# Optimization experiments

Measured on AMD Instinct MI355X. Metric: run time of the kernel, lower is better.

Reference implementation:

```python
import jax, jax.numpy as jnp
import numpy as np
import math

D_MODEL, H, D_FF = 1024, 16, 4096
B, S = 4, 2048
EPS = 1e-6

def layer_norm(x, alpha, beta):
    # Faithful to torch: x.std uses Bessel correction (ddof=1), eps added to std.
    mean = jnp.mean(x, axis=-1, keepdims=True)
    std = jnp.std(x, axis=-1, keepdims=True, ddof=1)
    return alpha * (x - mean) / (std + EPS) + beta

def setup_inputs() -> dict:
    key = jax.random.key(0)
    ks = jax.random.split(key, 8)
    sc = 0.02
    return {
        "x": jax.random.normal(ks[0], (B, S, D_MODEL), jnp.float32),
        "mask": jnp.ones((B, 1, 1, S), jnp.int32),
        "wq": jax.random.normal(ks[1], (D_MODEL, D_MODEL), jnp.float32) * sc,
        "wk": jax.random.normal(ks[2], (D_MODEL, D_MODEL), jnp.float32) * sc,
        "wv": jax.random.normal(ks[3], (D_MODEL, D_MODEL), jnp.float32) * sc,
        "wo": jax.random.normal(ks[4], (D_MODEL, D_MODEL), jnp.float32) * sc,
        "w1": jax.random.normal(ks[5], (D_MODEL, D_FF), jnp.float32) * sc,
        "b1": jnp.zeros((D_FF,), jnp.float32),
        "w2": jax.random.normal(ks[6], (D_FF, D_MODEL), jnp.float32) * sc,
        "b2": jnp.zeros((D_MODEL,), jnp.float32),
        "ln1_a": jnp.ones((D_MODEL,), jnp.float32),
        "ln1_b": jnp.zeros((D_MODEL,), jnp.float32),
        "ln2_a": jnp.ones((D_MODEL,), jnp.float32),
        "ln2_b": jnp.zeros((D_MODEL,), jnp.float32),
    }

def mha(xn, mask, wq, wk, wv, wo):
    b, s, d = xn.shape
    d_k = d // H
    q = (xn @ wq).reshape(b, s, H, d_k).transpose(0, 2, 1, 3)  # [B,H,S,dk]
    k = (xn @ wk).reshape(b, s, H, d_k).transpose(0, 2, 1, 3)
    v = (xn @ wv).reshape(b, s, H, d_k).transpose(0, 2, 1, 3)
    scores = jnp.einsum('bhqd,bhkd->bhqk', q, k) / math.sqrt(d_k)
    scores = jnp.where(mask == 0, -1e9, scores)
    attn = jax.nn.softmax(scores, axis=-1)
    out = jnp.einsum('bhqk,bhkd->bhqd', attn, v)
    out = out.transpose(0, 2, 1, 3).reshape(b, s, d)
    return out @ wo

def reference(x, mask, wq, wk, wv, wo, w1, b1, w2, b2, ln1_a, ln1_b, ln2_a, ln2_b):
    # Pre-LN residual 1: self-attention (dropout=0 / eval mode -> identity)
    xn = layer_norm(x, ln1_a, ln1_b)
    x = x + mha(xn, mask, wq, wk, wv, wo)
    # Pre-LN residual 2: FFN
    xn = layer_norm(x, ln2_a, ln2_b)
    ff = jax.nn.relu(xn @ w1 + b1) @ w2 + b2
    return x + ff
```

## Files before the change

### kernel.cpp

```cpp
#include <hip/hip_runtime.h>
#include <hip/hip_bf16.h>

typedef __bf16 bf16x8 __attribute__((ext_vector_type(8)));
typedef __bf16 bf16x4 __attribute__((ext_vector_type(4)));
typedef float  f32x4  __attribute__((ext_vector_type(4)));

#define MFMA(a, b, c) __builtin_amdgcn_mfma_f32_16x16x32_bf16((a), (b), (c), 0, 0, 0)

#define GLOAD16(gp, lp) __builtin_amdgcn_global_load_lds(                      \
    (const __attribute__((address_space(1))) void*)(gp),                       \
    (__attribute__((address_space(3))) void*)(lp), 16, 0, 0)

__device__ inline unsigned int pkbf(float a, float b) {
    __bf16 x = (__bf16)a, y = (__bf16)b;
    return (unsigned int)*(unsigned short*)&x |
           ((unsigned int)*(unsigned short*)&y << 16);
}

__global__ __launch_bounds__(256) void transpose_cvt(
    const float* __restrict__ src, __bf16* __restrict__ dst, int Kd, int Nd)
{
    __shared__ float tile[32][33];
    const int k0 = blockIdx.y * 32, n0 = blockIdx.x * 32;
    const int t = threadIdx.x;
    const int r = t >> 5, c = t & 31;
#pragma unroll
    for (int i = 0; i < 4; ++i)
        tile[r + i * 8][c] = src[(long)(k0 + r + i * 8) * Nd + n0 + c];
    __syncthreads();
#pragma unroll
    for (int i = 0; i < 4; ++i)
        dst[(long)(n0 + r + i * 8) * Kd + k0 + c] = (__bf16)tile[c][r + i * 8];
}

__global__ __launch_bounds__(256) void transpose_v(
    const __bf16* __restrict__ V, __bf16* __restrict__ Vt)
{
    __shared__ __bf16 tile[32][33];
    const int bh = blockIdx.z;
    const int s0 = blockIdx.x * 32, d0 = blockIdx.y * 32;
    const int t = threadIdx.x, r = t >> 5, c = t & 31;
    const __bf16* Vp = V + (long)bh * 2048 * 64;
    __bf16* Tp = Vt + (long)bh * 64 * 2048;
#pragma unroll
    for (int i = 0; i < 4; ++i)
        tile[r + i * 8][c] = Vp[(long)(s0 + r + i * 8) * 64 + d0 + c];
    __syncthreads();
#pragma unroll
    for (int i = 0; i < 4; ++i)
        Tp[(long)(d0 + r + i * 8) * 2048 + s0 + c] = tile[c][r + i * 8];
}

__global__ __launch_bounds__(256) void ln_kernel(
    const float* __restrict__ in, const float* __restrict__ ga,
    const float* __restrict__ gb, __bf16* __restrict__ out)
{
    const int row = blockIdx.x;
    const int t = threadIdx.x;
    const float4 xv = *(const float4*)(in + (long)row * 1024 + t * 4);
    float s  = xv.x + xv.y + xv.z + xv.w;
    float sq = xv.x * xv.x + xv.y * xv.y + xv.z * xv.z + xv.w * xv.w;
#pragma unroll
    for (int off = 32; off; off >>= 1) {
        s  += __shfl_xor(s, off);
        sq += __shfl_xor(sq, off);
    }
    __shared__ float red[8];
    const int w = t >> 6;
    if ((t & 63) == 0) { red[w * 2] = s; red[w * 2 + 1] = sq; }
    __syncthreads();
    s  = red[0] + red[2] + red[4] + red[6];
    sq = red[1] + red[3] + red[5] + red[7];
    const float mean = s * (1.0f / 1024.0f);
    const float var  = fmaxf((sq - s * mean) * (1.0f / 1023.0f), 0.0f);
    const float dinv = 1.0f / (sqrtf(var) + 1e-6f);
    const float4 av = *(const float4*)(ga + t * 4);
    const float4 bv = *(const float4*)(gb + t * 4);
    bf16x4 o;
    o[0] = (__bf16)((xv.x - mean) * dinv * av.x + bv.x);
    o[1] = (__bf16)((xv.y - mean) * dinv * av.y + bv.y);
    o[2] = (__bf16)((xv.z - mean) * dinv * av.z + bv.z);
    o[3] = (__bf16)((xv.w - mean) * dinv * av.w + bv.w);
    *(bf16x4*)(out + (long)row * 1024 + t * 4) = o;
}

template <int MODE>
__global__ __launch_bounds__(256) void gemm_bt(
    const __bf16* __restrict__ A, const __bf16* __restrict__ Bt,
    int M, int N, int K,
    const float* __restrict__ bias, const float* resid,
    float* outf, __bf16* __restrict__ outb,
    __bf16* __restrict__ qb, __bf16* __restrict__ kb, __bf16* __restrict__ vb)
{
    __shared__ __align__(16) __bf16 Alds[128 * 32];
    __shared__ __align__(16) __bf16 Blds[128 * 32];

    const int t = threadIdx.x;
    const int lane = t & 63, w = t >> 6;
    const int wr = w >> 1, wc = w & 1;
    const int g = lane >> 4, l15 = lane & 15;

    const int nwg = gridDim.x * gridDim.y;
    const int hwid = blockIdx.y * gridDim.x + blockIdx.x;
    const int wid = (hwid & 7) * (nwg >> 3) + (hwid >> 3);
    const int bm = (wid / gridDim.x) * 128;
    const int bn = (wid % gridDim.x) * 128;

    const int cr = t >> 2;
    const int cc = (t & 3) * 8;
    const __bf16* Ag  = A  + (long)(bm + cr) * K + cc;
    const __bf16* Ag2 = Ag + (long)64 * K;
    const __bf16* Bg  = Bt + (long)(bn + cr) * K + cc;
    const __bf16* Bg2 = Bg + (long)64 * K;
    char* Alp = (char*)Alds + t * 16;
    char* Blp = (char*)Blds + t * 16;

    f32x4 acc[4][4] = {};
    const int nk = K / 32;

    for (int kt = 0; kt < nk; ++kt) {
        const long ko = (long)kt * 32;
        __syncthreads();
        GLOAD16(Ag + ko,  Alp);
        GLOAD16(Ag2 + ko, Alp + 4096);
        GLOAD16(Bg + ko,  Blp);
        GLOAD16(Bg2 + ko, Blp + 4096);
        __syncthreads();
        bf16x8 af[4], bfr[4];
#pragma unroll
        for (int mi = 0; mi < 4; ++mi)
            af[mi] = *(const bf16x8*)(Alds + (wr * 64 + mi * 16 + l15) * 32 + g * 8);
#pragma unroll
        for (int ni = 0; ni < 4; ++ni)
            bfr[ni] = *(const bf16x8*)(Blds + (wc * 64 + ni * 16 + l15) * 32 + g * 8);
#pragma unroll
        for (int mi = 0; mi < 4; ++mi)
#pragma unroll
            for (int ni = 0; ni < 4; ++ni)
                acc[mi][ni] = MFMA(af[mi], bfr[ni], acc[mi][ni]);
    }

#pragma unroll
    for (int mi = 0; mi < 4; ++mi) {
#pragma unroll
        for (int ni = 0; ni < 4; ++ni) {
#pragma unroll
            for (int r = 0; r < 4; ++r) {
                const int gr = bm + wr * 64 + mi * 16 + g * 4 + r;
                const int gc = bn + wc * 64 + ni * 16 + l15;
                const float vacc = acc[mi][ni][r];
                if constexpr (MODE == 0) {
                    const int bufi = gc >> 10;
                    const int hd = gc & 1023;
                    const int h = hd >> 6, d = hd & 63;
                    const int b = gr >> 11, sx = gr & 2047;
                    __bf16* dst = (bufi == 0) ? qb : ((bufi == 1) ? kb : vb);
                    dst[((long)((b * 16 + h) * 2048 + sx)) * 64 + d] = (__bf16)vacc;
                } else if constexpr (MODE == 1) {
                    const long idx = (long)gr * N + gc;
                    outf[idx] = vacc + resid[idx];
                } else if constexpr (MODE == 2) {
                    const float y = fmaxf(vacc + bias[gc], 0.0f);
                    outb[(long)gr * N + gc] = (__bf16)y;
                } else {
                    const long idx = (long)gr * N + gc;
                    outf[idx] = vacc + bias[gc] + resid[idx];
                }
            }
        }
    }
}

__global__ __launch_bounds__(256, 2) void attn_kernel(
    const __bf16* __restrict__ Q, const __bf16* __restrict__ Kk,
    const __bf16* __restrict__ Vt, const int* __restrict__ mask,
    __bf16* __restrict__ O)
{
    __shared__ __align__(16) char Klds[8192];
    __shared__ __align__(16) char Vlds[8192];
    __shared__ int mlds[64];
    __shared__ int tflag[32];

    const int t = threadIdx.x;
    const int lane = t & 63, w = t >> 6;
    const int g = lane >> 4, l15 = lane & 15;
    const int bh = blockIdx.x >> 4;
    const int qt = blockIdx.x & 15;
    const int b = bh >> 4, h = bh & 15;
    const int q0 = qt * 128 + w * 32;

    const __bf16* Qp = Q  + (long)bh * 2048 * 64;
    const __bf16* Kp = Kk + (long)bh * 2048 * 64;
    const __bf16* Vp = Vt + (long)bh * 64 * 2048;
    const int* mp = mask + b * 2048;

    {
        const int4* mi4 = (const int4*)(mp + t * 8);
        const int4 ma = mi4[0], mb = mi4[1];
        const int ok = (ma.x && ma.y && ma.z && ma.w &&
                        mb.x && mb.y && mb.z && mb.w) ? 1 : 0;
        const unsigned long long bal = __ballot(ok);
        if ((lane & 7) == 0)
            tflag[t >> 3] = (((bal >> lane) & 0xFFull) == 0xFFull) ? 1 : 0;
    }

    bf16x8 qreg[2][2];
#pragma unroll
    for (int qf = 0; qf < 2; ++qf)
#pragma unroll
        for (int kh = 0; kh < 2; ++kh)
            qreg[qf][kh] = *(const bf16x8*)(Qp + (long)(q0 + qf * 16 + l15) * 64 + kh * 32 + g * 8);

    bf16x8 vone;
#pragma unroll
    for (int j = 0; j < 8; ++j) vone[j] = (__bf16)1.0f;

    const float Csc = 0.18033688011112042f;
    float m2_run[2] = {-1e30f, -1e30f};
    f32x4 la[2] = {};
    f32x4 ot[2][4] = {};

    const int sr0 = t >> 3;
    const int sce = (t & 7) * 8;
    const int swz0 = sr0 * 128 + (((t & 7) * 16) ^ ((sr0 & 7) << 4));
    const int swz1 = swz0 + 32 * 128;

    bf16x8 kr0 = *(const bf16x8*)(Kp + (long)sr0 * 64 + sce);
    bf16x8 kr1 = *(const bf16x8*)(Kp + (long)(sr0 + 32) * 64 + sce);
    bf16x8 vr0 = *(const bf16x8*)(Vp + (long)sr0 * 2048 + sce);
    bf16x8 vr1 = *(const bf16x8*)(Vp + (long)(sr0 + 32) * 2048 + sce);
    int mr = (t < 64) ? mp[t] : 0;

    for (int kc = 0; kc < 32; ++kc) {
        __syncthreads();
        *(bf16x8*)(Klds + swz0) = kr0;
        *(bf16x8*)(Klds + swz1) = kr1;
        *(bf16x8*)(Vlds + swz0) = vr0;
        *(bf16x8*)(Vlds + swz1) = vr1;
        if (t < 64) mlds[t] = mr;
        __syncthreads();
        if (kc < 31) {
            const int kv0 = (kc + 1) * 64;
            kr0 = *(const bf16x8*)(Kp + (long)(kv0 + sr0) * 64 + sce);
            kr1 = *(const bf16x8*)(Kp + (long)(kv0 + sr0 + 32) * 64 + sce);
            vr0 = *(const bf16x8*)(Vp + (long)sr0 * 2048 + kv0 + sce);
            vr1 = *(const bf16x8*)(Vp + (long)(sr0 + 32) * 2048 + kv0 + sce);
            if (t < 64) mr = mp[kv0 + t];
        }
        const bool fullv = (tflag[kc] != 0);

        bf16x8 kf[4][2];
#pragma unroll
        for (int f = 0; f < 4; ++f)
#pragma unroll
            for (int dh = 0; dh < 2; ++dh)
                kf[f][dh] = *(const bf16x8*)(Klds + (f * 16 + l15) * 128 +
                                             ((dh * 64 + g * 16) ^ ((l15 & 7) << 4)));
        f32x4 sf[2][4] = {};
        __builtin_amdgcn_s_setprio(1);
#pragma unroll
        for (int qf = 0; qf < 2; ++qf)
#pragma unroll
            for (int f = 0; f < 4; ++f) {
                sf[qf][f] = MFMA(kf[f][0], qreg[qf][0], sf[qf][f]);
                sf[qf][f] = MFMA(kf[f][1], qreg[qf][1], sf[qf][f]);
            }
        __builtin_amdgcn_s_setprio(0);

        bf16x8 av[4][2];
#pragma unroll
        for (int df = 0; df < 4; ++df) {
            const int row = (df * 16 + l15) * 128;
            const int sx = (l15 & 7) << 4;
#pragma unroll
            for (int hh = 0; hh < 2; ++hh) {
                const bf16x4 lo = *(const bf16x4*)(Vlds + row + ((hh * 64 + g * 8) ^ sx));
                const bf16x4 hi = *(const bf16x4*)(Vlds + row + ((hh * 64 + 32 + g * 8) ^ sx));
                bf16x8 a;
                a[0] = lo[0]; a[1] = lo[1]; a[2] = lo[2]; a[3] = lo[3];
                a[4] = hi[0]; a[5] = hi[1]; a[6] = hi[2]; a[7] = hi[3];
                av[df][hh] = a;
            }
        }

#pragma unroll
        for (int qf = 0; qf < 2; ++qf) {
            float s[16];
            if (fullv) {
#pragma unroll
                for (int i = 0; i < 16; ++i) s[i] = sf[qf][i >> 2][i & 3];
            } else {
                int mvv[16];
#pragma unroll
                for (int f = 0; f < 4; ++f) {
                    const int4 mq = *(const int4*)&mlds[f * 16 + g * 4];
                    mvv[f * 4 + 0] = mq.x; mvv[f * 4 + 1] = mq.y;
                    mvv[f * 4 + 2] = mq.z; mvv[f * 4 + 3] = mq.w;
                }
#pragma unroll
                for (int i = 0; i < 16; ++i)
                    s[i] = (mvv[i] == 0) ? -1e9f : sf[qf][i >> 2][i & 3];
            }
            float m01 = fmaxf(s[0], s[1]),   m23 = fmaxf(s[2], s[3]);
            float m45 = fmaxf(s[4], s[5]),   m67 = fmaxf(s[6], s[7]);
            float m89 = fmaxf(s[8], s[9]),   mab = fmaxf(s[10], s[11]);
            float mcd = fmaxf(s[12], s[13]), mef = fmaxf(s[14], s[15]);
            float mx = fmaxf(fmaxf(fmaxf(m01, m23), fmaxf(m45, m67)),
                             fmaxf(fmaxf(m89, mab), fmaxf(mcd, mef)));
            mx = fmaxf(mx, __shfl_xor(mx, 16));
            mx = fmaxf(mx, __shfl_xor(mx, 32));
            const float m2 = mx * Csc;
            if (!__all(m2 - m2_run[qf] <= 8.0f)) {
                const float m2n = fmaxf(m2_run[qf], m2);
                const float alpha = __builtin_amdgcn_exp2f(m2_run[qf] - m2n);
#pragma unroll
                for (int r = 0; r < 4; ++r) la[qf][r] *= alpha;
#pragma unroll
                for (int df = 0; df < 4; ++df)
#pragma unroll
                    for (int r = 0; r < 4; ++r) ot[qf][df][r] *= alpha;
                m2_run[qf] = m2n;
            }
            const float nm2 = -m2_run[qf];
            float p[16];
#pragma unroll
            for (int i = 0; i < 16; ++i)
                p[i] = __builtin_amdgcn_exp2f(__builtin_fmaf(s[i], Csc, nm2));

#pragma unroll
            for (int hh = 0; hh < 2; ++hh) {
                unsigned int pu[4] = {pkbf(p[hh * 8 + 0], p[hh * 8 + 1]),
                                      pkbf(p[hh * 8 + 2], p[hh * 8 + 3]),
                                      pkbf(p[hh * 8 + 4], p[hh * 8 + 5]),
                                      pkbf(p[hh * 8 + 6], p[hh * 8 + 7])};
                bf16x8 pf = *(bf16x8*)pu;
                __builtin_amdgcn_s_setprio(1);
#pragma unroll
                for (int df = 0; df < 4; ++df)
                    ot[qf][df] = MFMA(av[df][hh], pf, ot[qf][df]);
                la[qf] = MFMA(vone, pf, la[qf]);
                __builtin_amdgcn_s_setprio(0);
            }
        }
    }

#pragma unroll
    for (int qf = 0; qf < 2; ++qf) {
        const float inv = 1.0f / la[qf][0];
        const int q = q0 + qf * 16 + l15;
        __bf16* orow = O + (long)(b * 2048 + q) * 1024 + h * 64;
#pragma unroll
        for (int df = 0; df < 4; ++df)
#pragma unroll
            for (int rp = 0; rp < 2; ++rp) {
                const int d = df * 16 + g * 4 + rp * 2;
                *(unsigned int*)(orow + d) =
                    pkbf(ot[qf][df][rp * 2] * inv, ot[qf][df][rp * 2 + 1] * inv);
            }
    }
}

extern "C" void kernel_launch(void* const* d_in, const int* in_sizes, int n_in,
                              void* d_out, int out_size, void* d_ws, size_t ws_size,
                              hipStream_t stream)
{
    const float* x    = (const float*)d_in[0];
    const int*   mask = (const int*)  d_in[1];
    const float* wq   = (const float*)d_in[2];
    const float* wk   = (const float*)d_in[3];
    const float* wv   = (const float*)d_in[4];
    const float* wo   = (const float*)d_in[5];
    const float* w1   = (const float*)d_in[6];
    const float* b1   = (const float*)d_in[7];
    const float* w2   = (const float*)d_in[8];
    const float* b2   = (const float*)d_in[9];
    const float* l1a  = (const float*)d_in[10];
    const float* l1b  = (const float*)d_in[11];
    const float* l2a  = (const float*)d_in[12];
    const float* l2b  = (const float*)d_in[13];
    float* out = (float*)d_out;

    char* ws = (char*)d_ws;
    __bf16* wqkvT = (__bf16*)(ws);
    __bf16* woT   = (__bf16*)(ws + 6291456);
    __bf16* w1T   = (__bf16*)(ws + 8388608);
    __bf16* w2T   = (__bf16*)(ws + 16777216);
    __bf16* xn    = (__bf16*)(ws + 25165824);
    __bf16* Vtb   = (__bf16*)(ws + 25165824);
    __bf16* Qb    = (__bf16*)(ws + 41943040);
    __bf16* Kb    = (__bf16*)(ws + 58720256);
    __bf16* Vb    = (__bf16*)(ws + 75497472);
    __bf16* attO  = (__bf16*)(ws + 92274688);
    __bf16* ffh   = (__bf16*)(ws + 41943040);

    transpose_cvt<<<dim3(32, 32),  256, 0, stream>>>(wq, wqkvT,               1024, 1024);
    transpose_cvt<<<dim3(32, 32),  256, 0, stream>>>(wk, wqkvT + 1024 * 1024, 1024, 1024);
    transpose_cvt<<<dim3(32, 32),  256, 0, stream>>>(wv, wqkvT + 2048 * 1024, 1024, 1024);
    transpose_cvt<<<dim3(32, 32),  256, 0, stream>>>(wo, woT,                 1024, 1024);
    transpose_cvt<<<dim3(128, 32), 256, 0, stream>>>(w1, w1T,                 1024, 4096);
    transpose_cvt<<<dim3(32, 128), 256, 0, stream>>>(w2, w2T,                 4096, 1024);

    ln_kernel<<<8192, 256, 0, stream>>>(x, l1a, l1b, xn);
    gemm_bt<0><<<dim3(24, 64), 256, 0, stream>>>(xn, wqkvT, 8192, 3072, 1024,
                                                 nullptr, nullptr, nullptr, nullptr, Qb, Kb, Vb);
    transpose_v<<<dim3(64, 2, 64), 256, 0, stream>>>(Vb, Vtb);
    attn_kernel<<<1024, 256, 0, stream>>>(Qb, Kb, Vtb, mask, attO);
    gemm_bt<1><<<dim3(8, 64), 256, 0, stream>>>(attO, woT, 8192, 1024, 1024,
                                                nullptr, x, out, nullptr, nullptr, nullptr, nullptr);
    ln_kernel<<<8192, 256, 0, stream>>>(out, l2a, l2b, xn);
    gemm_bt<2><<<dim3(32, 64), 256, 0, stream>>>(xn, w1T, 8192, 4096, 1024,
                                                 b1, nullptr, nullptr, ffh, nullptr, nullptr, nullptr);
    gemm_bt<3><<<dim3(8, 64), 256, 0, stream>>>(ffh, w2T, 8192, 1024, 4096,
                                                b2, out, out, nullptr, nullptr, nullptr, nullptr);
    (void)in_sizes; (void)n_in; (void)out_size; (void)ws_size;
}
```

Measured before the change: 490.8 us.

## Double-buffer LDS tiles in GEMM and attention kernels with explicit waitcnt barriers

The GEMM main loop now uses two LDS buffers and prefetches tile kt+2 via global_load_lds while computing on the current tile. It uses explicit vmcnt/lgkmcnt waits and raw s_barrier in place of two __syncthreads per iteration, and raises wave priority around the MFMAs. The attention kernel also double-buffers its K/V/mask LDS tiles, so the next tile is written to the alternate buffer after compute, leaving one barrier per iteration. The goal is to overlap global memory latency with MFMA work and cut barrier stalls, at the cost of twice the LDS. That could lower occupancy, and the hand-written waitcnt logic is fragile.

Result: slower. 516.0 us (+5.1%).

```diff
diff --git a/kernel.cpp b/kernel.cpp
--- a/kernel.cpp
+++ b/kernel.cpp
@@ -10,6 +10,13 @@
 #define GLOAD16(gp, lp) __builtin_amdgcn_global_load_lds(                      \
     (const __attribute__((address_space(1))) void*)(gp),                       \
     (__attribute__((address_space(3))) void*)(lp), 16, 0, 0)
+
+#define WAITV4() asm volatile("s_waitcnt vmcnt(4)" ::: "memory")
+#define WAITV0() asm volatile("s_waitcnt vmcnt(0)" ::: "memory")
+#define WAITL()  asm volatile("s_waitcnt lgkmcnt(0)" ::: "memory")
+#define SBAR()   do { __builtin_amdgcn_sched_barrier(0);                       \
+                      __builtin_amdgcn_s_barrier();                            \
+                      __builtin_amdgcn_sched_barrier(0); } while (0)
 
 __device__ inline unsigned int pkbf(float a, float b) {
     __bf16 x = (__bf16)a, y = (__bf16)b;
@@ -92,8 +99,8 @@
     float* outf, __bf16* __restrict__ outb,
     __bf16* __restrict__ qb, __bf16* __restrict__ kb, __bf16* __restrict__ vb)
 {
-    __shared__ __align__(16) __bf16 Alds[128 * 32];
-    __shared__ __align__(16) __bf16 Blds[128 * 32];
+    __shared__ __align__(16) __bf16 Alds[2][128 * 32];
+    __shared__ __align__(16) __bf16 Blds[2][128 * 32];
 
     const int t = threadIdx.x;
     const int lane = t & 63, w = t >> 6;
@@ -112,33 +119,55 @@
     const __bf16* Ag2 = Ag + (long)64 * K;
     const __bf16* Bg  = Bt + (long)(bn + cr) * K + cc;
     const __bf16* Bg2 = Bg + (long)64 * K;
-    char* Alp = (char*)Alds + t * 16;
-    char* Blp = (char*)Blds + t * 16;
+    char* Alp = (char*)(&Alds[0][0]) + t * 16;
+    char* Blp = (char*)(&Blds[0][0]) + t * 16;
 
     f32x4 acc[4][4] = {};
     const int nk = K / 32;
 
+#define STAGE_T(kt, buf) do {                                                  \
+        const long ko_ = (long)(kt) * 32;                                      \
+        GLOAD16(Ag  + ko_, Alp + (buf) * 8192);                                \
+        GLOAD16(Ag2 + ko_, Alp + (buf) * 8192 + 4096);                         \
+        GLOAD16(Bg  + ko_, Blp + (buf) * 8192);                                \
+        GLOAD16(Bg2 + ko_, Blp + (buf) * 8192 + 4096); } while (0)
+
+    STAGE_T(0, 0);
+    STAGE_T(1, 1);
+    WAITV4();
+    SBAR();
+
     for (int kt = 0; kt < nk; ++kt) {
-        const long ko = (long)kt * 32;
-        __syncthreads();
-        GLOAD16(Ag + ko,  Alp);
-        GLOAD16(Ag2 + ko, Alp + 4096);
-        GLOAD16(Bg + ko,  Blp);
-        GLOAD16(Bg2 + ko, Blp + 4096);
-        __syncthreads();
+        const int cur = kt & 1;
+        const __bf16* Ab = &Alds[cur][0];
+        const __bf16* Bb = &Blds[cur][0];
         bf16x8 af[4], bfr[4];
 #pragma unroll
         for (int mi = 0; mi < 4; ++mi)
-            af[mi] = *(const bf16x8*)(Alds + (wr * 64 + mi * 16 + l15) * 32 + g * 8);
+            af[mi] = *(const bf16x8*)(Ab + (wr * 64 + mi * 16 + l15) * 32 + g * 8);
 #pragma unroll
         for (int ni = 0; ni < 4; ++ni)
-            bfr[ni] = *(const bf16x8*)(Blds + (wc * 64 + ni * 16 + l15) * 32 + g * 8);
+            bfr[ni] = *(const bf16x8*)(Bb + (wc * 64 + ni * 16 + l15) * 32 + g * 8);
+        __builtin_amdgcn_s_setprio(1);
 #pragma unroll
         for (int mi = 0; mi < 4; ++mi)
 #pragma unroll
             for (int ni = 0; ni < 4; ++ni)
                 acc[mi][ni] = MFMA(af[mi], bfr[ni], acc[mi][ni]);
-    }
+        __builtin_amdgcn_s_setprio(0);
+        WAITL();
+        SBAR();
+        if (kt + 1 < nk) {
+            if (kt + 2 < nk) {
+                STAGE_T(kt + 2, cur);
+                WAITV4();
+            } else {
+                WAITV0();
+            }
+            SBAR();
+        }
+    }
+#undef STAGE_T
 
 #pragma unroll
     for (int mi = 0; mi < 4; ++mi) {
@@ -176,9 +205,9 @@
     const __bf16* __restrict__ Vt, const int* __restrict__ mask,
     __bf16* __restrict__ O)
 {
-    __shared__ __align__(16) char Klds[8192];
-    __shared__ __align__(16) char Vlds[8192];
-    __shared__ int mlds[64];
+    __shared__ __align__(16) char Klds[2][8192];
+    __shared__ __align__(16) char Vlds[2][8192];
+    __shared__ int mlds[2][64];
     __shared__ int tflag[32];
 
     const int t = threadIdx.x;
@@ -230,23 +259,23 @@
     bf16x8 vr0 = *(const bf16x8*)(Vp + (long)sr0 * 2048 + sce);
     bf16x8 vr1 = *(const bf16x8*)(Vp + (long)(sr0 + 32) * 2048 + sce);
     int mr = (t < 64) ? mp[t] : 0;
+    *(bf16x8*)(Klds[0] + swz0) = kr0;
+    *(bf16x8*)(Klds[0] + swz1) = kr1;
+    *(bf16x8*)(Vlds[0] + swz0) = vr0;
+    *(bf16x8*)(Vlds[0] + swz1) = vr1;
+    if (t < 64) mlds[0][t] = mr;
+    kr0 = *(const bf16x8*)(Kp + (long)(64 + sr0) * 64 + sce);
+    kr1 = *(const bf16x8*)(Kp + (long)(64 + sr0 + 32) * 64 + sce);
+    vr0 = *(const bf16x8*)(Vp + (long)sr0 * 2048 + 64 + sce);
+    vr1 = *(const bf16x8*)(Vp + (long)(sr0 + 32) * 2048 + 64 + sce);
+    mr = (t < 64) ? mp[64 + t] : 0;
+    WAITL();
+    SBAR();
 
     for (int kc = 0; kc < 32; ++kc) {
-        __syncthreads();
-        *(bf16x8*)(Klds + swz0) = kr0;
-        *(bf16x8*)(Klds + swz1) = kr1;
-        *(bf16x8*)(Vlds + swz0) = vr0;
-        *(bf16x8*)(Vlds + swz1) = vr1;
-        if (t < 64) mlds[t] = mr;
-        __syncthreads();
-        if (kc < 31) {
-            const int kv0 = (kc + 1) * 64;
-            kr0 = *(const bf16x8*)(Kp + (long)(kv0 + sr0) * 64 + sce);
-            kr1 = *(const bf16x8*)(Kp + (long)(kv0 + sr0 + 32) * 64 + sce);
-            vr0 = *(const bf16x8*)(Vp + (long)sr0 * 2048 + kv0 + sce);
-            vr1 = *(const bf16x8*)(Vp + (long)(sr0 + 32) * 2048 + kv0 + sce);
-            if (t < 64) mr = mp[kv0 + t];
-        }
+        const int cur = kc & 1;
+        const char* Kc = Klds[cur];
+        const char* Vc = Vlds[cur];
         const bool fullv = (tflag[kc] != 0);
 
         bf16x8 kf[4][2];
@@ -254,7 +283,7 @@
         for (int f = 0; f < 4; ++f)
 #pragma unroll
             for (int dh = 0; dh < 2; ++dh)
-                kf[f][dh] = *(const bf16x8*)(Klds + (f * 16 + l15) * 128 +
+                kf[f][dh] = *(const bf16x8*)(Kc + (f * 16 + l15) * 128 +
                                              ((dh * 64 + g * 16) ^ ((l15 & 7) << 4)));
         f32x4 sf[2][4] = {};
         __builtin_amdgcn_s_setprio(1);
@@ -274,8 +303,8 @@
             const int sx = (l15 & 7) << 4;
 #pragma unroll
             for (int hh = 0; hh < 2; ++hh) {
-                const bf16x4 lo = *(const bf16x4*)(Vlds + row + ((hh * 64 + g * 8) ^ sx));
-                const bf16x4 hi = *(const bf16x4*)(Vlds + row + ((hh * 64 + 32 + g * 8) ^ sx));
+                const bf16x4 lo = *(const bf16x4*)(Vc + row + ((hh * 64 + g * 8) ^ sx));
+                const bf16x4 hi = *(const bf16x4*)(Vc + row + ((hh * 64 + 32 + g * 8) ^ sx));
                 bf16x8 a;
                 a[0] = lo[0]; a[1] = lo[1]; a[2] = lo[2]; a[3] = lo[3];
                 a[4] = hi[0]; a[5] = hi[1]; a[6] = hi[2]; a[7] = hi[3];
@@ -293,7 +322,7 @@
                 int mvv[16];
 #pragma unroll
                 for (int f = 0; f < 4; ++f) {
-                    const int4 mq = *(const int4*)&mlds[f * 16 + g * 4];
+                    const int4 mq = *(const int4*)&mlds[cur][f * 16 + g * 4];
                     mvv[f * 4 + 0] = mq.x; mvv[f * 4 + 1] = mq.y;
                     mvv[f * 4 + 2] = mq.z; mvv[f * 4 + 3] = mq.w;
                 }
@@ -342,6 +371,26 @@
                 __builtin_amdgcn_s_setprio(0);
             }
         }
+
+        if (kc < 31) {
+            char* Kn = Klds[cur ^ 1];
+            char* Vn = Vlds[cur ^ 1];
+            *(bf16x8*)(Kn + swz0) = kr0;
+            *(bf16x8*)(Kn + swz1) = kr1;
+            *(bf16x8*)(Vn + swz0) = vr0;
+            *(bf16x8*)(Vn + swz1) = vr1;
+            if (t < 64) mlds[cur ^ 1][t] = mr;
+            if (kc < 30) {
+                const int kv0 = (kc + 2) * 64;
+                kr0 = *(const bf16x8*)(Kp + (long)(kv0 + sr0) * 64 + sce);
+                kr1 = *(const bf16x8*)(Kp + (long)(kv0 + sr0 + 32) * 64 + sce);
+                vr0 = *(const bf16x8*)(Vp + (long)sr0 * 2048 + kv0 + sce);
+                vr1 = *(const bf16x8*)(Vp + (long)(sr0 + 32) * 2048 + kv0 + sce);
+                mr = (t < 64) ? mp[kv0 + t] : 0;
+            }
+            WAITL();
+        }
+        SBAR();
     }
 
 #pragma unroll
```

## Load attention K/V fragments directly from global memory, dropping LDS staging

Applied to the files above, without the earlier changes.

The attention kernel no longer stages K, V and mask tiles through shared memory with two barriers per key chunk. Each wave now loads its MFMA fragments straight from global memory and relies on L1/L2 for reuse across the four waves. Blocks are also remapped so that neighbouring block IDs fall on different batch-heads, and the occupancy hint in launch_bounds is dropped. The intent is to remove barrier stalls and LDS traffic, at the cost of more global and cache traffic, narrower 8-byte V loads, and no explicit prefetch.

New measurement: 701.9 us. +43.0%, slower.

```diff
diff --git a/kernel.cpp b/kernel.cpp
--- a/kernel.cpp
+++ b/kernel.cpp
@@ -171,21 +171,21 @@
     }
 }
 
-__global__ __launch_bounds__(256, 2) void attn_kernel(
+__global__ __launch_bounds__(256) void attn_kernel(
     const __bf16* __restrict__ Q, const __bf16* __restrict__ Kk,
     const __bf16* __restrict__ Vt, const int* __restrict__ mask,
     __bf16* __restrict__ O)
 {
-    __shared__ __align__(16) char Klds[8192];
-    __shared__ __align__(16) char Vlds[8192];
-    __shared__ int mlds[64];
     __shared__ int tflag[32];
 
     const int t = threadIdx.x;
     const int lane = t & 63, w = t >> 6;
     const int g = lane >> 4, l15 = lane & 15;
-    const int bh = blockIdx.x >> 4;
-    const int qt = blockIdx.x & 15;
+
+    const int bid = blockIdx.x;
+    const int idx = bid >> 3;
+    const int bh = (bid & 7) * 8 + (idx >> 4);
+    const int qt = idx & 15;
     const int b = bh >> 4, h = bh & 15;
     const int q0 = qt * 128 + w * 32;
 
@@ -203,6 +203,7 @@
         if ((lane & 7) == 0)
             tflag[t >> 3] = (((bal >> lane) & 0xFFull) == 0xFFull) ? 1 : 0;
     }
+    __syncthreads();
 
     bf16x8 qreg[2][2];
 #pragma unroll
@@ -220,42 +221,31 @@
     f32x4 la[2] = {};
     f32x4 ot[2][4] = {};
 
-    const int sr0 = t >> 3;
-    const int sce = (t & 7) * 8;
-    const int swz0 = sr0 * 128 + (((t & 7) * 16) ^ ((sr0 & 7) << 4));
-    const int swz1 = swz0 + 32 * 128;
-
-    bf16x8 kr0 = *(const bf16x8*)(Kp + (long)sr0 * 64 + sce);
-    bf16x8 kr1 = *(const bf16x8*)(Kp + (long)(sr0 + 32) * 64 + sce);
-    bf16x8 vr0 = *(const bf16x8*)(Vp + (long)sr0 * 2048 + sce);
-    bf16x8 vr1 = *(const bf16x8*)(Vp + (long)(sr0 + 32) * 2048 + sce);
-    int mr = (t < 64) ? mp[t] : 0;
+    const __bf16* kbase = Kp + (long)l15 * 64 + g * 8;
+    const __bf16* vbase = Vp + (long)l15 * 2048 + g * 4;
 
     for (int kc = 0; kc < 32; ++kc) {
-        __syncthreads();
-        *(bf16x8*)(Klds + swz0) = kr0;
-        *(bf16x8*)(Klds + swz1) = kr1;
-        *(bf16x8*)(Vlds + swz0) = vr0;
-        *(bf16x8*)(Vlds + swz1) = vr1;
-        if (t < 64) mlds[t] = mr;
-        __syncthreads();
-        if (kc < 31) {
-            const int kv0 = (kc + 1) * 64;
-            kr0 = *(const bf16x8*)(Kp + (long)(kv0 + sr0) * 64 + sce);
-            kr1 = *(const bf16x8*)(Kp + (long)(kv0 + sr0 + 32) * 64 + sce);
-            vr0 = *(const bf16x8*)(Vp + (long)sr0 * 2048 + kv0 + sce);
-            vr1 = *(const bf16x8*)(Vp + (long)(sr0 + 32) * 2048 + kv0 + sce);
-            if (t < 64) mr = mp[kv0 + t];
+        const int kv0 = kc * 64;
+        const bool fullv = (tflag[kc] != 0);
+
+        bf16x8 kf[4][2];
+#pragma unroll
+        for (int f = 0; f < 4; ++f)
+#pragma unroll
+            for (int dh = 0; dh < 2; ++dh)
+                kf[f][dh] = *(const bf16x8*)(kbase + (long)(kv0 + f * 16) * 64 + dh * 32);
+
+        bf16x4 avlo[4][2], avhi[4][2];
+#pragma unroll
+        for (int df = 0; df < 4; ++df) {
+            const __bf16* vrow = vbase + (long)(df * 16) * 2048 + kv0;
+#pragma unroll
+            for (int hh = 0; hh < 2; ++hh) {
+                avlo[df][hh] = *(const bf16x4*)(vrow + hh * 32);
+                avhi[df][hh] = *(const bf16x4*)(vrow + hh * 32 + 16);
+            }
         }
-        const bool fullv = (tflag[kc] != 0);
-
-        bf16x8 kf[4][2];
-#pragma unroll
-        for (int f = 0; f < 4; ++f)
-#pragma unroll
-            for (int dh = 0; dh < 2; ++dh)
-                kf[f][dh] = *(const bf16x8*)(Klds + (f * 16 + l15) * 128 +
-                                             ((dh * 64 + g * 16) ^ ((l15 & 7) << 4)));
+
         f32x4 sf[2][4] = {};
         __builtin_amdgcn_s_setprio(1);
 #pragma unroll
@@ -267,22 +257,6 @@
             }
         __builtin_amdgcn_s_setprio(0);
 
-        bf16x8 av[4][2];
-#pragma unroll
-        for (int df = 0; df < 4; ++df) {
-            const int row = (df * 16 + l15) * 128;
-            const int sx = (l15 & 7) << 4;
-#pragma unroll
-            for (int hh = 0; hh < 2; ++hh) {
-                const bf16x4 lo = *(const bf16x4*)(Vlds + row + ((hh * 64 + g * 8) ^ sx));
-                const bf16x4 hi = *(const bf16x4*)(Vlds + row + ((hh * 64 + 32 + g * 8) ^ sx));
-                bf16x8 a;
-                a[0] = lo[0]; a[1] = lo[1]; a[2] = lo[2]; a[3] = lo[3];
-                a[4] = hi[0]; a[5] = hi[1]; a[6] = hi[2]; a[7] = hi[3];
-                av[df][hh] = a;
-            }
-        }
-
 #pragma unroll
         for (int qf = 0; qf < 2; ++qf) {
             float s[16];
@@ -290,16 +264,14 @@
 #pragma unroll
                 for (int i = 0; i < 16; ++i) s[i] = sf[qf][i >> 2][i & 3];
             } else {
-                int mvv[16];
 #pragma unroll
                 for (int f = 0; f < 4; ++f) {
-                    const int4 mq = *(const int4*)&mlds[f * 16 + g * 4];
-                    mvv[f * 4 + 0] = mq.x; mvv[f * 4 + 1] = mq.y;
-                    mvv[f * 4 + 2] = mq.z; mvv[f * 4 + 3] = mq.w;
+                    const int4 mq = *(const int4*)(mp + kv0 + f * 16 + g * 4);
+                    s[f * 4 + 0] = (mq.x == 0) ? -1e9f : sf[qf][f][0];
+                    s[f * 4 + 1] = (mq.y == 0) ? -1e9f : sf[qf][f][1];
+                    s[f * 4 + 2] = (mq.z == 0) ? -1e9f : sf[qf][f][2];
+                    s[f * 4 + 3] = (mq.w == 0) ? -1e9f : sf[qf][f][3];
                 }
-#pragma unroll
-                for (int i = 0; i < 16; ++i)
-                    s[i] = (mvv[i] == 0) ? -1e9f : sf[qf][i >> 2][i & 3];
             }
             float m01 = fmaxf(s[0], s[1]),   m23 = fmaxf(s[2], s[3]);
             float m45 = fmaxf(s[4], s[5]),   m67 = fmaxf(s[6], s[7]);
@@ -336,8 +308,14 @@
                 bf16x8 pf = *(bf16x8*)pu;
                 __builtin_amdgcn_s_setprio(1);
 #pragma unroll
-                for (int df = 0; df < 4; ++df)
-                    ot[qf][df] = MFMA(av[df][hh], pf, ot[qf][df]);
+                for (int df = 0; df < 4; ++df) {
+                    bf16x8 a;
+                    a[0] = avlo[df][hh][0]; a[1] = avlo[df][hh][1];
+                    a[2] = avlo[df][hh][2]; a[3] = avlo[df][hh][3];
+                    a[4] = avhi[df][hh][0]; a[5] = avhi[df][hh][1];
+                    a[6] = avhi[df][hh][2]; a[7] = avhi[df][hh][3];
+                    ot[qf][df] = MFMA(a, pf, ot[qf][df]);
+                }
                 la[qf] = MFMA(vone, pf, la[qf]);
                 __builtin_amdgcn_s_setprio(0);
             }
```

## Double-buffer GEMM LDS tiles with register-staged global prefetch

Applied to the files above, without the earlier changes.

Replaces the direct global-to-LDS loads, which needed two barriers per K step, with register-staged prefetch into a double-buffered LDS tile. The loads for step kt+2 are issued while step kt computes, and the loop now has one barrier per iteration. The aim is to hide global memory latency behind MFMA work. In exchange it doubles LDS use, adds registers for staging, and routes data through VGPRs instead of the direct LDS load path.

Result: faster. 456.4 us (-7.0%).

```diff
diff --git a/kernel.cpp b/kernel.cpp
--- a/kernel.cpp
+++ b/kernel.cpp
@@ -6,10 +6,6 @@
 typedef float  f32x4  __attribute__((ext_vector_type(4)));
 
 #define MFMA(a, b, c) __builtin_amdgcn_mfma_f32_16x16x32_bf16((a), (b), (c), 0, 0, 0)
-
-#define GLOAD16(gp, lp) __builtin_amdgcn_global_load_lds(                      \
-    (const __attribute__((address_space(1))) void*)(gp),                       \
-    (__attribute__((address_space(3))) void*)(lp), 16, 0, 0)
 
 __device__ inline unsigned int pkbf(float a, float b) {
     __bf16 x = (__bf16)a, y = (__bf16)b;
@@ -92,8 +88,8 @@
     float* outf, __bf16* __restrict__ outb,
     __bf16* __restrict__ qb, __bf16* __restrict__ kb, __bf16* __restrict__ vb)
 {
-    __shared__ __align__(16) __bf16 Alds[128 * 32];
-    __shared__ __align__(16) __bf16 Blds[128 * 32];
+    __shared__ __align__(16) __bf16 Alds[2][128 * 32];
+    __shared__ __align__(16) __bf16 Blds[2][128 * 32];
 
     const int t = threadIdx.x;
     const int lane = t & 63, w = t >> 6;
@@ -112,32 +108,55 @@
     const __bf16* Ag2 = Ag + (long)64 * K;
     const __bf16* Bg  = Bt + (long)(bn + cr) * K + cc;
     const __bf16* Bg2 = Bg + (long)64 * K;
-    char* Alp = (char*)Alds + t * 16;
-    char* Blp = (char*)Blds + t * 16;
+    const int wof = cr * 32 + cc;
 
     f32x4 acc[4][4] = {};
     const int nk = K / 32;
 
+    bf16x8 ra0 = *(const bf16x8*)(Ag);
+    bf16x8 ra1 = *(const bf16x8*)(Ag2);
+    bf16x8 rb0 = *(const bf16x8*)(Bg);
+    bf16x8 rb1 = *(const bf16x8*)(Bg2);
+    *(bf16x8*)(&Alds[0][wof])           = ra0;
+    *(bf16x8*)(&Alds[0][wof + 64 * 32]) = ra1;
+    *(bf16x8*)(&Blds[0][wof])           = rb0;
+    *(bf16x8*)(&Blds[0][wof + 64 * 32]) = rb1;
+    ra0 = *(const bf16x8*)(Ag  + 32);
+    ra1 = *(const bf16x8*)(Ag2 + 32);
+    rb0 = *(const bf16x8*)(Bg  + 32);
+    rb1 = *(const bf16x8*)(Bg2 + 32);
+    __syncthreads();
+
     for (int kt = 0; kt < nk; ++kt) {
-        const long ko = (long)kt * 32;
-        __syncthreads();
-        GLOAD16(Ag + ko,  Alp);
-        GLOAD16(Ag2 + ko, Alp + 4096);
-        GLOAD16(Bg + ko,  Blp);
-        GLOAD16(Bg2 + ko, Blp + 4096);
-        __syncthreads();
+        const int cur = kt & 1;
+        if (kt + 1 < nk) {
+            *(bf16x8*)(&Alds[cur ^ 1][wof])           = ra0;
+            *(bf16x8*)(&Alds[cur ^ 1][wof + 64 * 32]) = ra1;
+            *(bf16x8*)(&Blds[cur ^ 1][wof])           = rb0;
+            *(bf16x8*)(&Blds[cur ^ 1][wof + 64 * 32]) = rb1;
+            if (kt + 2 < nk) {
+                const long ko = (long)(kt + 2) * 32;
+                ra0 = *(const bf16x8*)(Ag  + ko);
+                ra1 = *(const bf16x8*)(Ag2 + ko);
+                rb0 = *(const bf16x8*)(Bg  + ko);
+                rb1 = *(const bf16x8*)(Bg2 + ko);
+            }
+        }
+        const __bf16* Ab = &Alds[cur][0];
+        const __bf16* Bb = &Blds[cur][0];
         bf16x8 af[4], bfr[4];
 #pragma unroll
         for (int mi = 0; mi < 4; ++mi)
-            af[mi] = *(const bf16x8*)(Alds + (wr * 64 + mi * 16 + l15) * 32 + g * 8);
+            af[mi] = *(const bf16x8*)(Ab + (wr * 64 + mi * 16 + l15) * 32 + g * 8);
 #pragma unroll
         for (int ni = 0; ni < 4; ++ni)
-            bfr[ni] = *(const bf16x8*)(Blds + (wc * 64 + ni * 16 + l15) * 32 + g * 8);
+            bfr[ni] = *(const bf16x8*)(Bb + (wc * 64 + ni * 16 + l15) * 32 + g * 8);
 #pragma unroll
         for (int mi = 0; mi < 4; ++mi)
 #pragma unroll
             for (int ni = 0; ni < 4; ++ni)
                 acc[mi][ni] = MFMA(af[mi], bfr[ni], acc[mi][ni]);
+        __syncthreads();
     }
 
 #pragma unroll
```
